# Performance work log

Hardware: AMD Instinct MI355X
Metric: run time of the kernel (lower is better)

Reference implementation:

```python
import jax, jax.numpy as jnp
import numpy as np

# Model dims (match init_kwargs)
B, L, C = 4, 4096, 1024   # batch, seq_len, dim
M = 128                   # memory_dim
P = 4                     # n_persistent
S = 64                    # segment_size
H = 8                     # num_heads in nn.MultiheadAttention


def _ln(x, g, b, eps=1e-5):
    mu = jnp.mean(x, -1, keepdims=True)
    var = jnp.mean((x - mu) ** 2, -1, keepdims=True)
    return (x - mu) * jax.lax.rsqrt(var + eps) * g + b


def setup_inputs() -> dict:
    key = jax.random.key(0)
    ks = jax.random.split(key, 16)
    def n(k, shape, s=0.02):
        return jax.random.normal(k, shape, jnp.float32) * s
    return {
        "x": jax.random.normal(ks[0], (B, L, C), jnp.float32),
        "persistent_memory": n(ks[1], (1, P, C)),
        "Wq": n(ks[2], (C, C)),            # query_proj (no bias)
        "Wk": n(ks[3], (C, C)),            # key_proj (no bias)
        "Wv": n(ks[4], (C, C)),            # value_proj (no bias)
        # NeuralMemoryModule.memory_net: Linear(C->M), SiLU, LN(M), Linear(M->M), LN(M)
        "mem_W1": n(ks[5], (M, C)), "mem_b1": jnp.zeros((M,)),
        "mem_ln1_g": jnp.ones((M,)), "mem_ln1_b": jnp.zeros((M,)),
        "mem_W2": n(ks[6], (M, M)), "mem_b2": jnp.zeros((M,)),
        "mem_ln2_g": jnp.ones((M,)), "mem_ln2_b": jnp.zeros((M,)),
        "mem_out_W": n(ks[7], (C, M)), "mem_out_b": jnp.zeros((C,)),
        "memory_state": jnp.zeros((1, M)),  # persistent buffer (zeros at init)
        # nn.MultiheadAttention in/out projections
        "mha_Wq": n(ks[8], (C, C)), "mha_bq": jnp.zeros((C,)),
        "mha_Wk": n(ks[9], (C, C)), "mha_bk": jnp.zeros((C,)),
        "mha_Wv": n(ks[10], (C, C)), "mha_bv": jnp.zeros((C,)),
        "mha_Wo": n(ks[11], (C, C)), "mha_bo": jnp.zeros((C,)),
        "gn_g": jnp.ones((C,)), "gn_b": jnp.zeros((C,)),   # gate_norm
        "gate_W": n(ks[12], (C, C)), "gate_b": jnp.zeros((C,)),
        "out_W": n(ks[13], (C, C)), "out_b": jnp.zeros((C,)),
    }


def reference(x, persistent_memory, Wq, Wk, Wv,
              mem_W1, mem_b1, mem_ln1_g, mem_ln1_b,
              mem_W2, mem_b2, mem_ln2_g, mem_ln2_b,
              mem_out_W, mem_out_b, memory_state,
              mha_Wq, mha_bq, mha_Wk, mha_bk, mha_Wv, mha_bv, mha_Wo, mha_bo,
              gn_g, gn_b, gate_W, gate_b, out_W, out_b):
    Bx, Lx, Cx = x.shape
    n_seg = Lx // S
    # Eval-mode: memory_state is frozen, so all segments are independent ->
    # process every segment in parallel instead of a Python loop over L.
    xs = x.reshape(Bx * n_seg, S, Cx)           # [N, S, C]
    q_seg = xs @ Wq.T                            # query_proj
    # retrieve from long-term memory: memory_net(queries) + memory_state -> output_proj
    h = jax.nn.silu(q_seg @ mem_W1.T + mem_b1)
    h = _ln(h, mem_ln1_g, mem_ln1_b)
    h = h @ mem_W2.T + mem_b2
    h = _ln(h, mem_ln2_g, mem_ln2_b)             # [N, S, M]
    retrieved = (h + memory_state[0]) @ mem_out_W.T + mem_out_b  # [N, S, C]
    # context = [retrieved_memory, persistent_memory, current_segment]
    pm = jnp.broadcast_to(persistent_memory, (Bx * n_seg, P, Cx))
    context = jnp.concatenate([retrieved, pm, xs], axis=1)       # [N, T, C], T=S+P+S
    k_in = context @ Wk.T
    v_in = context @ Wv.T
    T = context.shape[1]
    hd = Cx // H
    q = (q_seg @ mha_Wq.T + mha_bq).reshape(-1, S, H, hd)
    k = (k_in @ mha_Wk.T + mha_bk).reshape(-1, T, H, hd)
    v = (v_in @ mha_Wv.T + mha_bv).reshape(-1, T, H, hd)
    scores = jnp.einsum('nshd,nthd->nhst', q, k) / jnp.sqrt(jnp.float32(hd))
    attn = jnp.einsum('nhst,nthd->nshd', jax.nn.softmax(scores, -1), v)
    attn = attn.reshape(-1, S, Cx) @ mha_Wo.T + mha_bo           # [N, S, C]
    # learned gate blend + output projection
    gate = jax.nn.sigmoid(_ln(attn, gn_g, gn_b) @ gate_W.T + gate_b)
    out = (gate * attn + xs) @ out_W.T + out_b
    return out.reshape(Bx, Lx, Cx)
```

## Files before the change

### kernel.cpp

```cpp
#include <hip/hip_runtime.h>
#include <hip/hip_bf16.h>
#include <math.h>


using bf16 = __hip_bfloat16;

typedef __attribute__((ext_vector_type(8))) short bf16x8;
typedef __attribute__((ext_vector_type(4))) float f32x4;

__device__ __forceinline__ float ldf(const bf16* p) { return __bfloat162float(*p); }
__device__ __forceinline__ float ldf(const float* p) { return *p; }
__device__ __forceinline__ void stf(bf16* p, float v) { *p = __float2bfloat16(v); }
__device__ __forceinline__ void stf(float* p, float v) { *p = v; }
__device__ __forceinline__ float b2f(const bf16& b) { return __bfloat162float(b); }
__device__ __forceinline__ float bsf(short s) {
  union { unsigned u; float f; } cv;
  cv.u = (unsigned)(unsigned short)s << 16;
  return cv.f;
}

enum { ACT_NONE = 0, ACT_SILU = 1, ACT_SIGMOID = 2, ACT_GATE = 3, ACT_PSILU = 4 };

__global__ void detect_kernel(const unsigned short* g, int* flag) {
  if (threadIdx.x == 0) *flag = (g[0] != 0) ? 1 : 0;
}

struct ConvArgs {
  const void* src[29];
  bf16* dst[29];
  int n[29];
  int bstart[30];
};

__global__ __launch_bounds__(256) void convall_kernel(ConvArgs a, const int* __restrict__ flag) {
  int b = blockIdx.x;
  int ti = 0;
  while (ti < 28 && b >= a.bstart[ti + 1]) ++ti;
  int i = (b - a.bstart[ti]) * 256 + threadIdx.x;
  if (i >= a.n[ti]) return;
  if (*flag) a.dst[ti][i] = ((const bf16*)a.src[ti])[i];
  else a.dst[ti][i] = __float2bfloat16(((const float*)a.src[ti])[i]);
}

__global__ __launch_bounds__(256) void conv_kernel(
    const void* __restrict__ src, bf16* __restrict__ dst, int n, size_t src_off,
    const int* __restrict__ flag) {
  int i = (blockIdx.x * 256 + threadIdx.x) * 8;
  if (i >= n) return;
  if (*flag) {
    *(uint4*)((unsigned short*)dst + i) =
        *(const uint4*)((const unsigned short*)src + src_off + i);
  } else {
    const float* s = (const float*)src + src_off + i;
    const float4 a = *(const float4*)s;
    const float4 b = *(const float4*)(s + 4);
    bf16 t[8] = {__float2bfloat16(a.x), __float2bfloat16(a.y),
                 __float2bfloat16(a.z), __float2bfloat16(a.w),
                 __float2bfloat16(b.x), __float2bfloat16(b.y),
                 __float2bfloat16(b.z), __float2bfloat16(b.w)};
    *(uint4*)((unsigned short*)dst + i) = *(const uint4*)t;
  }
}

__global__ __launch_bounds__(256) void pack_bias4(
    const bf16* __restrict__ bk, const bf16* __restrict__ bv,
    const bf16* __restrict__ bq, const bf16* __restrict__ b1,
    bf16* __restrict__ o) {
  int j = blockIdx.x * 256 + threadIdx.x;
  if (j >= 3200) return;
  float v;
  if (j < 1024) v = b2f(bk[j]);
  else if (j < 2048) v = b2f(bv[j - 1024]);
  else if (j < 3072) v = b2f(bq[j - 2048]);
  else v = b2f(b1[j - 3072]);
  o[j] = __float2bfloat16(v);
}

__global__ __launch_bounds__(256) void transpose_kernel(
    const bf16* __restrict__ srcb, bf16* __restrict__ dstb, int rows, int cols) {
  __shared__ unsigned short t[64][72];
  const unsigned short* src = (const unsigned short*)srcb;
  unsigned short* dst = (unsigned short*)dstb;
  const int r0 = blockIdx.y * 64, c0 = blockIdx.x * 64;
  for (int e = threadIdx.x; e < 64 * 8; e += 256) {
    int r = e >> 3, c8 = e & 7;
    uint4 v = *(const uint4*)(src + (size_t)(r0 + r) * cols + c0 + c8 * 8);
    *(uint4*)&t[r][c8 * 8] = v;
  }
  __syncthreads();
  for (int e = threadIdx.x; e < 64 * 8; e += 256) {
    int c = e >> 3, r8 = (e & 7) * 8;
    unsigned short v[8];
#pragma unroll
    for (int j = 0; j < 8; ++j) v[j] = t[r8 + j][c];
    *(uint4*)(dst + (size_t)(c0 + c) * rows + r0 + r8) = *(uint4*)v;
  }
}

__global__ __launch_bounds__(256) void kpvp_kernel(
    const bf16* __restrict__ pmb, const bf16* __restrict__ mobb,
    const bf16* __restrict__ Wb, const bf16* __restrict__ bias4b,
    bf16* __restrict__ kp, bf16* __restrict__ vp, bf16* __restrict__ bkv)
{
  const short* pm = (const short*)pmb;
  const short* mob = (const short*)mobb;
  const short* W = (const short*)Wb;
  const int wave = threadIdx.x >> 6, lane = threadIdx.x & 63;
  const int c = blockIdx.x * 4 + wave;
  const short* wrow = W + (size_t)c * 1024 + lane * 16;
  const bf16x8 w0 = *(const bf16x8*)wrow;
  const bf16x8 w1 = *(const bf16x8*)(wrow + 8);
  float acc[5];
#pragma unroll
  for (int m = 0; m < 5; ++m) {
    const short* prow = (m < 4) ? (pm + m * 1024 + lane * 16) : (mob + lane * 16);
    const bf16x8 p0 = *(const bf16x8*)prow;
    const bf16x8 p1 = *(const bf16x8*)(prow + 8);
    float s = 0.f;
#pragma unroll
    for (int j = 0; j < 8; ++j) s += bsf(w0[j]) * bsf(p0[j]) + bsf(w1[j]) * bsf(p1[j]);
    acc[m] = s;
  }
#pragma unroll
  for (int d = 1; d < 64; d <<= 1) {
#pragma unroll
    for (int m = 0; m < 5; ++m) acc[m] += __shfl_xor(acc[m], d);
  }
  if (lane == 0) {
    const float bv = b2f(bias4b[c]);
    bf16* dst = (c < 1024) ? (kp + c) : (vp + (c - 1024));
#pragma unroll
    for (int m = 0; m < 4; ++m) stf(dst + m * 1024, acc[m] + bv);
    stf(&bkv[c], acc[4] + bv);
  }
}

__device__ __forceinline__ void gl_lds16(const short* g, short* l) {
  __builtin_amdgcn_global_load_lds(
      (const __attribute__((address_space(1))) void*)g,
      (__attribute__((address_space(3))) void*)l, 16, 0, 0);
}

template <typename TC, int ACT, bool HAS_BIAS>
__global__ __launch_bounds__(256) void mgemm(
    const bf16* __restrict__ Ab, const bf16* __restrict__ Bw,
    const bf16* __restrict__ bias, TC* __restrict__ C,
    int M, int N, int K, int lda, int ldc,
    const bf16* __restrict__ ao, const void* __restrict__ xsrc, size_t xoff,
    const int* __restrict__ flag, int pn)
{
  __shared__ short As[2][128 * 32];
  __shared__ short Bs[2][128 * 32];
  const short* A = (const short*)Ab;
  const short* B = (const short*)Bw;
  const int tid = threadIdx.x;
  const int m0 = blockIdx.x * 128, n0 = blockIdx.y * 128;
  const int wave = tid >> 6, lane = tid & 63;
  const int wm = (wave & 1) * 64, wn = (wave >> 1) * 64;
  const int fm = lane & 15;
  const int fq = lane >> 4;
  const int fks = (fq ^ ((fm >> 1) & 3)) * 8;

  const int srow = tid >> 2;
  const int scol = ((tid & 3) ^ ((tid >> 3) & 3)) * 8;
  const short* gA0 = A + (size_t)(m0 + srow) * lda + scol;
  const short* gA1 = A + (size_t)(m0 + 64 + srow) * lda + scol;
  const short* gB0 = B + (size_t)(n0 + srow) * K + scol;
  const short* gB1 = B + (size_t)(n0 + 64 + srow) * K + scol;

  f32x4 acc[4][4] = {};
  const int NT = K >> 5;

#define STAGE(buf, k0)                              \
  do {                                              \
    gl_lds16(gA0 + (k0), &As[buf][tid * 8]);        \
    gl_lds16(gA1 + (k0), &As[buf][(256 + tid) * 8]);\
    gl_lds16(gB0 + (k0), &Bs[buf][tid * 8]);        \
    gl_lds16(gB1 + (k0), &Bs[buf][(256 + tid) * 8]);\
  } while (0)

  STAGE(0, 0);
  STAGE(1, 32);

  for (int kt = 0; kt < NT; ++kt) {
    const int cur = kt & 1;
    if (kt == NT - 1) asm volatile("s_waitcnt vmcnt(0)" ::: "memory");
    else              asm volatile("s_waitcnt vmcnt(4)" ::: "memory");
    __builtin_amdgcn_s_barrier();
    bf16x8 af[4], bfr[4];
#pragma unroll
    for (int i = 0; i < 4; ++i)
      af[i] = *(const bf16x8*)&As[cur][(wm + i * 16 + fm) * 32 + fks];
#pragma unroll
    for (int j = 0; j < 4; ++j)
      bfr[j] = *(const bf16x8*)&Bs[cur][(wn + j * 16 + fm) * 32 + fks];
#pragma unroll
    for (int i = 0; i < 4; ++i)
#pragma unroll
      for (int j = 0; j < 4; ++j)
        acc[i][j] = __builtin_amdgcn_mfma_f32_16x16x32_bf16(af[i], bfr[j], acc[i][j], 0, 0, 0);
    asm volatile("s_waitcnt lgkmcnt(0)" ::: "memory");
    __builtin_amdgcn_s_barrier();
    if (kt + 2 < NT) STAGE(cur, (kt + 2) * 32);
  }
#undef STAGE

  const int rg = fq * 4;
#pragma unroll
  for (int i = 0; i < 4; ++i) {
#pragma unroll
    for (int j = 0; j < 4; ++j) {
      const int n = n0 + wn + j * 16 + fm;
      float bv = 0.f;
      if (HAS_BIAS) bv = b2f(bias[n]);
#pragma unroll
      for (int r = 0; r < 4; ++r) {
        const int m = m0 + wm + i * 16 + rg + r;
        float v = acc[i][j][r] + bv;
        if (ACT == ACT_SILU) v = v / (1.f + __expf(-v));
        if (ACT == ACT_PSILU) { if (n >= pn) v = v / (1.f + __expf(-v)); }
        if (ACT == ACT_SIGMOID) v = 1.f / (1.f + __expf(-v));
        if (ACT == ACT_GATE) {
          v = 1.f / (1.f + __expf(-v));
          const size_t e = (size_t)m * 1024 + n;
          const float xv = *flag ? b2f(((const bf16*)xsrc)[xoff + e])
                                 : ((const float*)xsrc)[xoff + e];
          v = v * b2f(ao[e]) + xv;
        }
        stf(&C[(size_t)m * ldc + n], v);
      }
    }
  }
}

__global__ __launch_bounds__(256) void kgemm(
    const bf16* __restrict__ Ab, const bf16* __restrict__ Bw,
    float* __restrict__ P, int M, int N, int K, int lda)
{
  __shared__ short As[128 * 32];
  __shared__ short Bs[128 * 32];
  const short* A = (const short*)Ab;
  const short* B = (const short*)Bw;
  const int tid = threadIdx.x;
  const int m0 = blockIdx.x * 128, n0 = blockIdx.y * 128;
  const int kb = blockIdx.z * (K >> 2), ke = kb + (K >> 2);
  const int wave = tid >> 6, lane = tid & 63;
  const int wm = (wave & 1) * 64, wn = (wave >> 1) * 64;
  const int fm = lane & 15;
  const int fk = (lane >> 4) * 8;

  const int srow = tid >> 2, scol = (tid & 3) * 8;
  const short* gA0 = A + (size_t)(m0 + srow) * lda + scol;
  const short* gA1 = A + (size_t)(m0 + 64 + srow) * lda + scol;
  const short* gB0 = B + (size_t)(n0 + srow) * K + scol;
  const short* gB1 = B + (size_t)(n0 + 64 + srow) * K + scol;
  short* lA0 = As + tid * 8;
  short* lA1 = As + (256 + tid) * 8;
  short* lB0 = Bs + tid * 8;
  short* lB1 = Bs + (256 + tid) * 8;

  f32x4 acc[4][4] = {};

  for (int k0 = kb; k0 < ke; k0 += 32) {
    gl_lds16(gA0 + k0, lA0);
    gl_lds16(gA1 + k0, lA1);
    gl_lds16(gB0 + k0, lB0);
    gl_lds16(gB1 + k0, lB1);
    __syncthreads();
    bf16x8 af[4], bfr[4];
#pragma unroll
    for (int i = 0; i < 4; ++i)
      af[i] = *(const bf16x8*)&As[(wm + i * 16 + fm) * 32 + fk];
#pragma unroll
    for (int j = 0; j < 4; ++j)
      bfr[j] = *(const bf16x8*)&Bs[(wn + j * 16 + fm) * 32 + fk];
#pragma unroll
    for (int i = 0; i < 4; ++i)
#pragma unroll
      for (int j = 0; j < 4; ++j)
        acc[i][j] = __builtin_amdgcn_mfma_f32_16x16x32_bf16(af[i], bfr[j], acc[i][j], 0, 0, 0);
    __syncthreads();
  }

  float* Cp = P + (size_t)blockIdx.z * ((size_t)M * N);
  const int rg = (lane >> 4) * 4;
#pragma unroll
  for (int i = 0; i < 4; ++i)
#pragma unroll
    for (int j = 0; j < 4; ++j) {
      const int n = n0 + wn + j * 16 + fm;
#pragma unroll
      for (int r = 0; r < 4; ++r) {
        const int m = m0 + wm + i * 16 + rg + r;
        Cp[(size_t)m * N + n] = acc[i][j][r];
      }
    }
}

__global__ __launch_bounds__(256) void foldfin_kernel(
    const float* __restrict__ P, bf16* __restrict__ o, int MN) {
  int i = blockIdx.x * 256 + threadIdx.x;
  if (i >= MN) return;
  float s = P[i] + P[i + (size_t)MN] + P[i + 2 * (size_t)MN] + P[i + 3 * (size_t)MN];
  o[i] = __float2bfloat16(s);
}

template <typename TI, typename TO, bool ADD, int W, int BS>
__global__ __launch_bounds__(BS) void ln_kernel(
    const TI* __restrict__ in, const bf16* __restrict__ g, const bf16* __restrict__ b,
    const bf16* __restrict__ addv, TO* __restrict__ out, int ldin)
{
  __shared__ float red[BS];
  const int row = blockIdx.x;
  const TI* rin = in + (size_t)row * ldin;
  TO* rout = out + (size_t)row * W;
  const int NP = W / BS;
  float v[NP];
  float s = 0.f;
#pragma unroll
  for (int i = 0; i < NP; ++i) { v[i] = ldf(&rin[threadIdx.x + i * BS]); s += v[i]; }
  red[threadIdx.x] = s; __syncthreads();
  for (int o = BS / 2; o > 0; o >>= 1) {
    if (threadIdx.x < o) red[threadIdx.x] += red[threadIdx.x + o];
    __syncthreads();
  }
  const float mean = red[0] / W;
  __syncthreads();
  float sq = 0.f;
#pragma unroll
  for (int i = 0; i < NP; ++i) { float d = v[i] - mean; sq += d * d; }
  red[threadIdx.x] = sq; __syncthreads();
  for (int o = BS / 2; o > 0; o >>= 1) {
    if (threadIdx.x < o) red[threadIdx.x] += red[threadIdx.x + o];
    __syncthreads();
  }
  const float rstd = rsqrtf(red[0] / W + 1e-5f);
#pragma unroll
  for (int i = 0; i < NP; ++i) {
    int c = threadIdx.x + i * BS;
    float o_ = (v[i] - mean) * rstd * b2f(g[c]) + b2f(b[c]);
    if (ADD) o_ += b2f(addv[c]);
    stf(&rout[c], o_);
  }
}

__global__ __launch_bounds__(512) void attn_kernel(
    const bf16* __restrict__ qg, int str_q,
    const bf16* __restrict__ krv, int str_r,
    const bf16* __restrict__ kxv, int str_x, const bf16* __restrict__ kpg,
    const bf16* __restrict__ vpg, bf16* __restrict__ outg)
{
  __shared__ short qs[4 * 64 * 32];
  __shared__ short ksl[4 * 144 * 32];
  __shared__ short vt[128 * 168];
  __shared__ short pl[64 * 168];

  const int tid = threadIdx.x;
  unsigned bid = blockIdx.x;
  {
    const unsigned nwg = gridDim.x;
    const unsigned q_ = nwg >> 3, r_ = nwg & 7;
    const unsigned xcd = bid & 7, loc = bid >> 3;
    bid = (xcd < r_ ? xcd * (q_ + 1) : r_ * (q_ + 1) + (xcd - r_) * q_) + loc;
  }
  const int seg = (int)(bid >> 3), h = (int)(bid & 7);
  const unsigned short* q = (const unsigned short*)qg + (size_t)seg * 64 * str_q + h * 128;
  const unsigned short* kv_r = (const unsigned short*)krv + (size_t)seg * 64 * str_r + h * 128;
  const unsigned short* kv_x = (const unsigned short*)kxv + (size_t)seg * 64 * str_x + h * 128;
  const unsigned short* kp = (const unsigned short*)kpg;
  const unsigned short* vp = (const unsigned short*)vpg;
  const size_t obase = (size_t)seg * 64 * 1024 + h * 128;

  for (int ch = tid; ch < 64 * 16; ch += 512) {
    int row = ch >> 4, k8 = ch & 15;
    uint4 v = *(const uint4*)(q + (size_t)row * str_q + k8 * 8);
    *(uint4*)&qs[((k8 >> 2) * 64 + row) * 32 + (k8 & 3) * 8] = v;
  }
  for (int ch = tid; ch < 132 * 16; ch += 512) {
    int t = ch >> 4, k8 = ch & 15;
    const unsigned short* src;
    if (t < 64) src = kv_r + (size_t)t * str_r;
    else if (t < 68) src = kp + (size_t)(t - 64) * 1024 + h * 128;
    else src = kv_x + (size_t)(t - 68) * str_x;
    uint4 v = *(const uint4*)(src + k8 * 8);
    *(uint4*)&ksl[((k8 >> 2) * 144 + t) * 32 + (k8 & 3) * 8] = v;
  }
  __syncthreads();

  const int wave = tid >> 6, lane = tid & 63;
  const int fm = lane & 15, fq = lane >> 4;

  if (wave < 4) {
    const int s0 = wave * 16;
    f32x4 acc[10];
#pragma unroll
    for (int tt = 0; tt < 10; ++tt) acc[tt] = (f32x4){0.f, 0.f, 0.f, 0.f};
#pragma unroll
    for (int kb = 0; kb < 4; ++kb) {
      const bf16x8 a = *(const bf16x8*)&qs[(kb * 64 + s0 + fm) * 32 + fq * 8];
#pragma unroll
      for (int tt = 0; tt < 9; ++tt) {
        const bf16x8 b = *(const bf16x8*)&ksl[(kb * 144 + tt * 16 + fm) * 32 + fq * 8];
        acc[tt] = __builtin_amdgcn_mfma_f32_16x16x32_bf16(a, b, acc[tt], 0, 0, 0);
      }
    }
    const float scale = 0.08838834764831845f;
#pragma unroll
    for (int r = 0; r < 4; ++r) {
      float m = -3.0e38f;
#pragma unroll
      for (int tt = 0; tt < 9; ++tt) {
        int t = tt * 16 + fm;
        if (t < 132) m = fmaxf(m, acc[tt][r] * scale);
      }
      for (int d = 1; d < 16; d <<= 1) m = fmaxf(m, __shfl_xor(m, d));
      float e[10];
      float sum = 0.f;
#pragma unroll
      for (int tt = 0; tt < 10; ++tt) {
        int t = tt * 16 + fm;
        float ev = 0.f;
        if (t < 132) ev = __expf(acc[tt][r] * scale - m);
        e[tt] = ev; sum += ev;
      }
      for (int d = 1; d < 16; d <<= 1) sum += __shfl_xor(sum, d);
      const float inv = 1.f / sum;
      const int s = s0 + fq * 4 + r;
#pragma unroll
      for (int tt = 0; tt < 10; ++tt) {
        bf16 pv = __float2bfloat16(e[tt] * inv);
        pl[s * 168 + tt * 16 + fm] = *(const short*)&pv;
      }
    }
  } else {
    for (int ch = tid - 256; ch < 132 * 32; ch += 256) {
      int t = ch >> 5, d4 = (ch & 31) * 4;
      const unsigned short* src;
      if (t < 64) src = kv_r + 1024 + (size_t)t * str_r;
      else if (t < 68) src = vp + (size_t)(t - 64) * 1024 + h * 128;
      else src = kv_x + 1024 + (size_t)(t - 68) * str_x;
      uint2 w = *(const uint2*)(src + d4);
      vt[(d4 + 0) * 168 + t] = (short)(w.x & 0xffffu);
      vt[(d4 + 1) * 168 + t] = (short)(w.x >> 16);
      vt[(d4 + 2) * 168 + t] = (short)(w.y & 0xffffu);
      vt[(d4 + 3) * 168 + t] = (short)(w.y >> 16);
    }
    for (int ch = tid - 256; ch < 128 * 32; ch += 256) {
      int d = ch >> 5, tp = 132 + (ch & 31);
      vt[d * 168 + tp] = 0;
    }
  }
  __syncthreads();

  const int dt = wave;
  bf16x8 af[5];
#pragma unroll
  for (int kb = 0; kb < 5; ++kb)
    af[kb] = *(const bf16x8*)&vt[(dt * 16 + fm) * 168 + kb * 32 + fq * 8];
#pragma unroll
  for (int st = 0; st < 4; ++st) {
    f32x4 o = (f32x4){0.f, 0.f, 0.f, 0.f};
#pragma unroll
    for (int kb = 0; kb < 5; ++kb) {
      const bf16x8 bp = *(const bf16x8*)&pl[(st * 16 + fm) * 168 + kb * 32 + fq * 8];
      o = __builtin_amdgcn_mfma_f32_16x16x32_bf16(af[kb], bp, o, 0, 0, 0);
    }
    const int s = st * 16 + fm;
    bf16 b0 = __float2bfloat16(o[0]), b1 = __float2bfloat16(o[1]);
    bf16 b2 = __float2bfloat16(o[2]), b3 = __float2bfloat16(o[3]);
    uint2 w;
    w.x = ((unsigned)(*(unsigned short*)&b1) << 16) | (*(unsigned short*)&b0);
    w.y = ((unsigned)(*(unsigned short*)&b3) << 16) | (*(unsigned short*)&b2);
    *(uint2*)((unsigned short*)outg + obase + (size_t)s * 1024 + dt * 16 + fq * 4) = w;
  }
}

extern "C" void kernel_launch(void* const* d_in, const int* in_sizes, int n_in,
                              void* d_out, int out_size, void* d_ws, size_t ws_size,
                              hipStream_t stream)
{
  (void)n_in; (void)out_size;
  const int R = 16384, Cd = 1024;

  char* ws = (char*)d_ws;
  size_t off = 0;
  auto alloc = [&](size_t bytes) -> void* {
    void* p = ws + off;
    off += (bytes + 255) & ~(size_t)255;
    return p;
  };

  int* flag = (int*)alloc(256);
  bf16* W4    = (bf16*)alloc((size_t)3200 * Cd * sizeof(bf16));
  bf16* bias4 = (bf16*)alloc(3200 * sizeof(bf16));
  bf16* T     = (bf16*)alloc((size_t)Cd * Cd * sizeof(bf16));
  bf16* Wc    = (bf16*)alloc((size_t)2048 * 128 * sizeof(bf16));
  bf16* kp    = (bf16*)alloc((size_t)4 * Cd * sizeof(bf16));
  bf16* vp    = (bf16*)alloc((size_t)4 * Cd * sizeof(bf16));
  bf16* bkv   = (bf16*)alloc(2048 * sizeof(bf16));
  bf16* WqStk = (bf16*)alloc((size_t)1152 * Cd * sizeof(bf16));
  bf16* nb[30];
  nb[0] = nullptr;
  for (int i = 1; i < 30; ++i) nb[i] = (bf16*)alloc((size_t)in_sizes[i] * sizeof(bf16));
  nb[16] = WqStk;
  nb[5]  = WqStk + (size_t)1024 * Cd;
  const size_t fixed_end = off;

  size_t avail = (ws_size > fixed_end + (1u << 20)) ? (ws_size - fixed_end - (1u << 20)) : 0;
  int crmax = (int)(avail / 17152);
  if (crmax > R) crmax = R;
  if (crmax < 128) crmax = 128;
  int nch = (R + crmax - 1) / crmax;
  int CR = ((R / nch + 127) / 128) * 128;
  while (CR * nch < R) CR += 128;

  const size_t chunk_start = off;
  const size_t RB = (size_t)CR * Cd * sizeof(bf16);
  bf16* Xc  = (bf16*)alloc(RB);
  bf16* QS4 = (bf16*)alloc((size_t)CR * 3200 * sizeof(bf16));
  bf16* h1b = (bf16*)alloc((size_t)CR * 128 * sizeof(bf16));
  bf16* h2b = (bf16*)alloc((size_t)CR * 128 * sizeof(bf16));
  bf16* Bb  = (bf16*)alloc(RB);
  bf16* KVr = (bf16*)alloc(2 * RB);
  bf16* Cc  = (bf16*)alloc(RB);
  const size_t chunk_bytes = off - chunk_start;

  dim3 blk(256);
  auto g128 = [](int M_, int N_) { return dim3((unsigned)(M_ / 128), (unsigned)(N_ / 128)); };

  detect_kernel<<<1, 64, 0, stream>>>((const unsigned short*)d_in[24], flag);
  {
    ConvArgs a;
    int bs = 0;
    for (int i = 1; i < 30; ++i) {
      a.src[i - 1] = d_in[i];
      a.dst[i - 1] = nb[i];
      a.n[i - 1] = in_sizes[i];
      a.bstart[i - 1] = bs;
      bs += (in_sizes[i] + 255) / 256;
    }
    a.bstart[29] = bs;
    convall_kernel<<<dim3((unsigned)bs), blk, 0, stream>>>(a, flag);
  }
  const bf16 *pm = nb[1], *Wq = nb[2], *Wk = nb[3], *Wv = nb[4];
  const bf16 *mem_W1 = nb[5], *mem_b1 = nb[6], *ln1g = nb[7], *ln1b = nb[8];
  const bf16 *mem_W2 = nb[9], *mem_b2 = nb[10], *ln2g = nb[11], *ln2b = nb[12];
  const bf16 *mem_oW = nb[13], *mem_ob = nb[14], *mstate = nb[15];
  const bf16 *mhaWq = nb[16], *mhabq = nb[17], *mhaWk = nb[18], *mhabk = nb[19];
  const bf16 *mhaWv = nb[20], *mhabv = nb[21], *mhaWo = nb[22], *mhabo = nb[23];
  const bf16 *gn_g = nb[24], *gn_b = nb[25], *gateW = nb[26], *gateb = nb[27];
  const bf16 *outW = nb[28], *outb = nb[29];
  bf16* Wkk = W4;
  bf16* Wvv = W4 + (size_t)1024 * Cd;
  bf16* Wqq = W4 + (size_t)2048 * Cd;
  bf16* Wm1 = W4 + (size_t)3072 * Cd;

  const bool use_ks = chunk_bytes >= (size_t)4 * 1152 * 1024 * sizeof(float);
  if (use_ks) {
    float* P = (float*)Xc;
    transpose_kernel<<<dim3(16, 16), blk, 0, stream>>>(Wq, T, 1024, 1024);
    kgemm<<<dim3(9, 8, 4), blk, 0, stream>>>(WqStk, T, P, 1152, 1024, 1024, 1024);
    foldfin_kernel<<<dim3(4608), blk, 0, stream>>>(P, Wqq, 1152 * 1024);
    transpose_kernel<<<dim3(16, 16), blk, 0, stream>>>(Wk, T, 1024, 1024);
    kgemm<<<dim3(8, 8, 4), blk, 0, stream>>>(mhaWk, T, P, 1024, 1024, 1024, 1024);
    foldfin_kernel<<<dim3(4096), blk, 0, stream>>>(P, Wkk, 1024 * 1024);
    transpose_kernel<<<dim3(16, 16), blk, 0, stream>>>(Wv, T, 1024, 1024);
    kgemm<<<dim3(8, 8, 4), blk, 0, stream>>>(mhaWv, T, P, 1024, 1024, 1024, 1024);
    foldfin_kernel<<<dim3(4096), blk, 0, stream>>>(P, Wvv, 1024 * 1024);
    transpose_kernel<<<dim3(2, 16), blk, 0, stream>>>(mem_oW, T, 1024, 128);
    kgemm<<<dim3(16, 1, 4), blk, 0, stream>>>(W4, T, P, 2048, 128, 1024, 1024);
    foldfin_kernel<<<dim3(1024), blk, 0, stream>>>(P, Wc, 2048 * 128);
  } else {
    transpose_kernel<<<dim3(16, 16), blk, 0, stream>>>(Wq, T, 1024, 1024);
    mgemm<bf16, ACT_NONE, false><<<g128(1024, 1024), blk, 0, stream>>>(
        mhaWq, T, nullptr, Wqq, 1024, 1024, 1024, 1024, 1024, nullptr, nullptr, 0, nullptr, 0);
    mgemm<bf16, ACT_NONE, false><<<g128(128, 1024), blk, 0, stream>>>(
        mem_W1, T, nullptr, Wm1, 128, 1024, 1024, 1024, 1024, nullptr, nullptr, 0, nullptr, 0);
    transpose_kernel<<<dim3(16, 16), blk, 0, stream>>>(Wk, T, 1024, 1024);
    mgemm<bf16, ACT_NONE, false><<<g128(1024, 1024), blk, 0, stream>>>(
        mhaWk, T, nullptr, Wkk, 1024, 1024, 1024, 1024, 1024, nullptr, nullptr, 0, nullptr, 0);
    transpose_kernel<<<dim3(16, 16), blk, 0, stream>>>(Wv, T, 1024, 1024);
    mgemm<bf16, ACT_NONE, false><<<g128(1024, 1024), blk, 0, stream>>>(
        mhaWv, T, nullptr, Wvv, 1024, 1024, 1024, 1024, 1024, nullptr, nullptr, 0, nullptr, 0);
    transpose_kernel<<<dim3(2, 16), blk, 0, stream>>>(mem_oW, T, 1024, 128);
    mgemm<bf16, ACT_NONE, false><<<g128(2048, 128), blk, 0, stream>>>(
        W4, T, nullptr, Wc, 2048, 128, 1024, 1024, 128, nullptr, nullptr, 0, nullptr, 0);
  }
  pack_bias4<<<13, blk, 0, stream>>>(mhabk, mhabv, mhabq, mem_b1, bias4);
  kpvp_kernel<<<dim3(512), blk, 0, stream>>>(pm, mem_ob, W4, bias4, kp, vp, bkv);

  for (int r0 = 0; r0 < R; r0 += CR) {
    const int cr = (R - r0 < CR) ? (R - r0) : CR;
    const int n = cr * Cd;
    conv_kernel<<<dim3((n / 8 + 255) / 256), blk, 0, stream>>>(
        d_in[0], Xc, n, (size_t)r0 * Cd, flag);

    mgemm<bf16, ACT_PSILU, true><<<g128(cr, 3200), blk, 0, stream>>>(
        Xc, W4, bias4, QS4, cr, 3200, 1024, 1024, 3200, nullptr, nullptr, 0, nullptr, 3072);

    ln_kernel<bf16, bf16, false, 128, 128><<<cr, 128, 0, stream>>>(
        QS4 + 3072, ln1g, ln1b, nullptr, h2b, 3200);
    mgemm<bf16, ACT_NONE, true><<<g128(cr, 128), blk, 0, stream>>>(
        h2b, mem_W2, mem_b2, h1b, cr, 128, 128, 128, 128, nullptr, nullptr, 0, nullptr, 0);
    ln_kernel<bf16, bf16, true, 128, 128><<<cr, 128, 0, stream>>>(h1b, ln2g, ln2b, mstate, h2b, 128);
    mgemm<bf16, ACT_NONE, true><<<g128(cr, 2048), blk, 0, stream>>>(
        h2b, Wc, bkv, KVr, cr, 2048, 128, 128, 2048, nullptr, nullptr, 0, nullptr, 0);

    attn_kernel<<<dim3((cr / 64) * 8), dim3(512), 0, stream>>>(
        QS4 + 2048, 3200, KVr, 2048, QS4, 3200, kp, vp, Xc);

    mgemm<bf16, ACT_NONE, true><<<g128(cr, Cd), blk, 0, stream>>>(
        Xc, mhaWo, mhabo, Bb, cr, Cd, Cd, Cd, Cd, nullptr, nullptr, 0, nullptr, 0);
    ln_kernel<bf16, bf16, false, 1024, 256><<<cr, 256, 0, stream>>>(Bb, gn_g, gn_b, nullptr, Cc, Cd);
    mgemm<bf16, ACT_GATE, true><<<g128(cr, Cd), blk, 0, stream>>>(
        Cc, gateW, gateb, Xc, cr, Cd, Cd, Cd, Cd, Bb, d_in[0], (size_t)r0 * Cd, flag, 0);
    mgemm<float, ACT_NONE, true><<<g128(cr, Cd), blk, 0, stream>>>(
        Xc, outW, outb, (float*)d_out + (size_t)r0 * Cd, cr, Cd, Cd, Cd, Cd,
        nullptr, nullptr, 0, nullptr, 0);
  }
}
```

Baseline: 878.7 us.

## Add 256x128 triple-buffered MFMA GEMM for the large per-chunk projections

Adds a new tgemm kernel for the four large per-chunk GEMMs: the fused QKV/memory projection, the MHA output projection, the gate and the output projection. It uses 512 threads and 256x128 output tiles, with 64-wide K steps. Loads go straight from global memory into XOR-swizzled LDS through a three-stage buffer, and MFMA issue priority is raised with s_setprio. The aim is more data reuse per tile, better hiding of load latency and fewer LDS bank conflicts than the 128x128 mgemm. In exchange it uses about 144KB of static LDS per block, which limits occupancy, and it falls back to mgemm when the chunk rows are not a multiple of 256.

```diff
diff --git a/kernel.cpp b/kernel.cpp
--- a/kernel.cpp
+++ b/kernel.cpp
@@ -233,6 +233,112 @@
   }
 }
 
+template <typename TC, int ACT, bool HAS_BIAS>
+__global__ __launch_bounds__(512, 2) void tgemm(
+    const bf16* __restrict__ Ab, const bf16* __restrict__ Bw,
+    const bf16* __restrict__ bias, TC* __restrict__ C,
+    int M, int N, int K, int lda, int ldc,
+    const bf16* __restrict__ ao, const void* __restrict__ xsrc, size_t xoff,
+    const int* __restrict__ flag, int pn)
+{
+  __shared__ short LA[3][256 * 64];
+  __shared__ short LB[3][128 * 64];
+  const short* A = (const short*)Ab;
+  const short* B = (const short*)Bw;
+  const int tid = threadIdx.x;
+  const int m0 = blockIdx.x * 256, n0 = blockIdx.y * 128;
+  const int wave = tid >> 6, lane = tid & 63;
+  const int wm = (wave & 1) * 128;
+  const int wn = (wave >> 1) * 32;
+  const int fm = lane & 15;
+  const int fq = lane >> 4;
+
+  const int srowA = tid >> 3;
+  const int sgrp = ((tid & 7) ^ ((tid >> 3) & 7)) * 8;
+  const short* tA0 = A + (size_t)(m0 + srowA) * lda + sgrp;
+  const short* tA1 = A + (size_t)(m0 + 64 + srowA) * lda + sgrp;
+  const short* tA2 = A + (size_t)(m0 + 128 + srowA) * lda + sgrp;
+  const short* tA3 = A + (size_t)(m0 + 192 + srowA) * lda + sgrp;
+  const short* tB0 = B + (size_t)(n0 + srowA) * K + sgrp;
+  const short* tB1 = B + (size_t)(n0 + 64 + srowA) * K + sgrp;
+
+  f32x4 acc[8][2] = {};
+  const int NT = K >> 6;
+
+#define TSTAGE(buf, t)                                   \
+  do {                                                   \
+    const int k0_ = (t) * 64;                            \
+    gl_lds16(tA0 + k0_, &LA[buf][tid * 8]);              \
+    gl_lds16(tA1 + k0_, &LA[buf][4096 + tid * 8]);       \
+    gl_lds16(tA2 + k0_, &LA[buf][8192 + tid * 8]);       \
+    gl_lds16(tA3 + k0_, &LA[buf][12288 + tid * 8]);      \
+    gl_lds16(tB0 + k0_, &LB[buf][tid * 8]);              \
+    gl_lds16(tB1 + k0_, &LB[buf][4096 + tid * 8]);       \
+  } while (0)
+
+  TSTAGE(0, 0);
+  TSTAGE(1, 1);
+  asm volatile("s_waitcnt vmcnt(6)" ::: "memory");
+  __builtin_amdgcn_s_barrier();
+
+  for (int t = 0; t < NT; ++t) {
+    const int buf = t % 3;
+    if (t + 2 < NT) TSTAGE((t + 2) % 3, t + 2);
+    const short* la = &LA[buf][0];
+    const short* lb = &LB[buf][0];
+#pragma unroll
+    for (int kk = 0; kk < 2; ++kk) {
+      const int sw = ((kk * 4 + fq) ^ (fm & 7)) * 8;
+      bf16x8 af[8], bfr[2];
+#pragma unroll
+      for (int mi = 0; mi < 8; ++mi)
+        af[mi] = *(const bf16x8*)&la[(wm + mi * 16 + fm) * 64 + sw];
+#pragma unroll
+      for (int nj = 0; nj < 2; ++nj)
+        bfr[nj] = *(const bf16x8*)&lb[(wn + nj * 16 + fm) * 64 + sw];
+      __builtin_amdgcn_s_setprio(1);
+#pragma unroll
+      for (int mi = 0; mi < 8; ++mi)
+#pragma unroll
+        for (int nj = 0; nj < 2; ++nj)
+          acc[mi][nj] = __builtin_amdgcn_mfma_f32_16x16x32_bf16(af[mi], bfr[nj], acc[mi][nj], 0, 0, 0);
+      __builtin_amdgcn_s_setprio(0);
+    }
+    if (t + 1 < NT) {
+      if (t + 2 < NT) asm volatile("s_waitcnt vmcnt(6)" ::: "memory");
+      else            asm volatile("s_waitcnt vmcnt(0)" ::: "memory");
+      __builtin_amdgcn_s_barrier();
+    }
+  }
+#undef TSTAGE
+
+#pragma unroll
+  for (int mi = 0; mi < 8; ++mi) {
+#pragma unroll
+    for (int nj = 0; nj < 2; ++nj) {
+      const int n = n0 + wn + nj * 16 + fm;
+      float bv = 0.f;
+      if (HAS_BIAS) bv = b2f(bias[n]);
+#pragma unroll
+      for (int r = 0; r < 4; ++r) {
+        const int m = m0 + wm + mi * 16 + fq * 4 + r;
+        float v = acc[mi][nj][r] + bv;
+        if (ACT == ACT_SILU) v = v / (1.f + __expf(-v));
+        if (ACT == ACT_PSILU) { if (n >= pn) v = v / (1.f + __expf(-v)); }
+        if (ACT == ACT_SIGMOID) v = 1.f / (1.f + __expf(-v));
+        if (ACT == ACT_GATE) {
+          v = 1.f / (1.f + __expf(-v));
+          const size_t e = (size_t)m * 1024 + n;
+          const float xv = *flag ? b2f(((const bf16*)xsrc)[xoff + e])
+                                 : ((const float*)xsrc)[xoff + e];
+          v = v * b2f(ao[e]) + xv;
+        }
+        stf(&C[(size_t)m * ldc + n], v);
+      }
+    }
+  }
+}
+
 __global__ __launch_bounds__(256) void kgemm(
     const bf16* __restrict__ Ab, const bf16* __restrict__ Bw,
     float* __restrict__ P, int M, int N, int K, int lda)
@@ -527,6 +633,7 @@
 
   dim3 blk(256);
   auto g128 = [](int M_, int N_) { return dim3((unsigned)(M_ / 128), (unsigned)(N_ / 128)); };
+  auto g256 = [](int M_, int N_) { return dim3((unsigned)(M_ / 256), (unsigned)(N_ / 128)); };
 
   detect_kernel<<<1, 64, 0, stream>>>((const unsigned short*)d_in[24], flag);
   {
@@ -592,11 +699,16 @@
   for (int r0 = 0; r0 < R; r0 += CR) {
     const int cr = (R - r0 < CR) ? (R - r0) : CR;
     const int n = cr * Cd;
+    const bool big = (cr % 256) == 0;
     conv_kernel<<<dim3((n / 8 + 255) / 256), blk, 0, stream>>>(
         d_in[0], Xc, n, (size_t)r0 * Cd, flag);
 
-    mgemm<bf16, ACT_PSILU, true><<<g128(cr, 3200), blk, 0, stream>>>(
-        Xc, W4, bias4, QS4, cr, 3200, 1024, 1024, 3200, nullptr, nullptr, 0, nullptr, 3072);
+    if (big)
+      tgemm<bf16, ACT_PSILU, true><<<g256(cr, 3200), dim3(512), 0, stream>>>(
+          Xc, W4, bias4, QS4, cr, 3200, 1024, 1024, 3200, nullptr, nullptr, 0, nullptr, 3072);
+    else
+      mgemm<bf16, ACT_PSILU, true><<<g128(cr, 3200), blk, 0, stream>>>(
+          Xc, W4, bias4, QS4, cr, 3200, 1024, 1024, 3200, nullptr, nullptr, 0, nullptr, 3072);
 
     ln_kernel<bf16, bf16, false, 128, 128><<<cr, 128, 0, stream>>>(
         QS4 + 3072, ln1g, ln1b, nullptr, h2b, 3200);
@@ -609,13 +721,25 @@
     attn_kernel<<<dim3((cr / 64) * 8), dim3(512), 0, stream>>>(
         QS4 + 2048, 3200, KVr, 2048, QS4, 3200, kp, vp, Xc);
 
-    mgemm<bf16, ACT_NONE, true><<<g128(cr, Cd), blk, 0, stream>>>(
-        Xc, mhaWo, mhabo, Bb, cr, Cd, Cd, Cd, Cd, nullptr, nullptr, 0, nullptr, 0);
+    if (big)
+      tgemm<bf16, ACT_NONE, true><<<g256(cr, Cd), dim3(512), 0, stream>>>(
+          Xc, mhaWo, mhabo, Bb, cr, Cd, Cd, Cd, Cd, nullptr, nullptr, 0, nullptr, 0);
+    else
+      mgemm<bf16, ACT_NONE, true><<<g128(cr, Cd), blk, 0, stream>>>(
+          Xc, mhaWo, mhabo, Bb, cr, Cd, Cd, Cd, Cd, nullptr, nullptr, 0, nullptr, 0);
     ln_kernel<bf16, bf16, false, 1024, 256><<<cr, 256, 0, stream>>>(Bb, gn_g, gn_b, nullptr, Cc, Cd);
-    mgemm<bf16, ACT_GATE, true><<<g128(cr, Cd), blk, 0, stream>>>(
-        Cc, gateW, gateb, Xc, cr, Cd, Cd, Cd, Cd, Bb, d_in[0], (size_t)r0 * Cd, flag, 0);
-    mgemm<float, ACT_NONE, true><<<g128(cr, Cd), blk, 0, stream>>>(
-        Xc, outW, outb, (float*)d_out + (size_t)r0 * Cd, cr, Cd, Cd, Cd, Cd,
-        nullptr, nullptr, 0, nullptr, 0);
-  }
-}
+    if (big) {
+      tgemm<bf16, ACT_GATE, true><<<g256(cr, Cd), dim3(512), 0, stream>>>(
+          Cc, gateW, gateb, Xc, cr, Cd, Cd, Cd, Cd, Bb, d_in[0], (size_t)r0 * Cd, flag, 0);
+      tgemm<float, ACT_NONE, true><<<g256(cr, Cd), dim3(512), 0, stream>>>(
+          Xc, outW, outb, (float*)d_out + (size_t)r0 * Cd, cr, Cd, Cd, Cd, Cd,
+          nullptr, nullptr, 0, nullptr, 0);
+    } else {
+      mgemm<bf16, ACT_GATE, true><<<g128(cr, Cd), blk, 0, stream>>>(
+          Cc, gateW, gateb, Xc, cr, Cd, Cd, Cd, Cd, Bb, d_in[0], (size_t)r0 * Cd, flag, 0);
+      mgemm<float, ACT_NONE, true><<<g128(cr, Cd), blk, 0, stream>>>(
+          Xc, outW, outb, (float*)d_out + (size_t)r0 * Cd, cr, Cd, Cd, Cd, Cd,
+          nullptr, nullptr, 0, nullptr, 0);
+    }
+  }
+}
```

Result: no change. 878.3 us (-0.1%).
